# Optimization experiments

Measured on AMD Instinct MI355X. Metric: run time of the kernel, lower is better.

The kernel has to match this reference:

```python
import jax, jax.numpy as jnp
import numpy as np
from jax import lax

EPOCHS = 3
N_IN, N_OUT = 20, 18
BN_EPS = 1e-5
RECT_EPS = 1e-4
TRIU = np.triu_indices(N_OUT)  # SPDVectorize upper-triangular indices


def _orth(key, n, m):
    # Stiefel init: orthonormal columns, like nn.init.orthogonal_
    q, _ = jnp.linalg.qr(jax.random.normal(key, (n, m), dtype=jnp.float32))
    return q


def setup_inputs() -> dict:
    key = jax.random.key(0)
    ks = jax.random.split(key, 8)
    bs = 2048
    f32 = jnp.float32
    return dict(
        x=jax.random.normal(ks[0], (bs, 1, 22, 438), dtype=f32),
        W1=jax.random.normal(ks[1], (22, 1, 22, 1), dtype=f32) * 0.1,
        b1=jnp.zeros((22,), f32),
        g1=jnp.ones((22,), f32), be1=jnp.zeros((22,), f32),
        W2=jax.random.normal(ks[2], (20, 22, 1, 12), dtype=f32) * 0.05,
        b2=jnp.zeros((20,), f32),
        g2=jnp.ones((20,), f32), be2=jnp.zeros((20,), f32),
        Wq=_orth(ks[3], N_IN, N_OUT),
        Wk=_orth(ks[4], N_IN, N_OUT),
        Wv=_orth(ks[5], N_IN, N_OUT),
        Wl=jax.random.normal(ks[6], (N_OUT * (N_OUT + 1) // 2 * EPOCHS, 4), dtype=f32) * 0.02,
        bl=jnp.zeros((4,), f32),
    )


def _bn(x, g, b):
    # BatchNorm2d forward in training mode (batch statistics, biased var)
    mean = x.mean(axis=(0, 2, 3), keepdims=True)
    var = ((x - mean) ** 2).mean(axis=(0, 2, 3), keepdims=True)
    return (x - mean) * lax.rsqrt(var + BN_EPS) * g[None, :, None, None] + b[None, :, None, None]


def _conv(x, w, b, pad_w):
    y = lax.conv_general_dilated(x, w, (1, 1), [(0, 0), (pad_w, pad_w)],
                                 dimension_numbers=('NCHW', 'OIHW', 'NCHW'))
    return y + b[None, :, None, None]


def _signal2spd(x):
    # x: (bs, C, L) -> trace-normalized covariance + 1e-5 * I
    L = x.shape[-1]
    xc = x - x.mean(-1, keepdims=True)
    cov = jnp.einsum('bcl,bdl->bcd', xc, xc) / (L - 1)
    cov = cov / jnp.trace(cov, axis1=-2, axis2=-1)[:, None, None]
    return cov + 1e-5 * jnp.eye(cov.shape[-1], dtype=cov.dtype)


def _patch_lens(n, epochs):
    base = n // epochs
    lens = [base] * epochs
    for i in range(n - base * epochs):
        lens[i] += 1
    return lens


def _spd_fn(t, fn):
    # SPD functional calculus via eigh (== torch.svd on SPD input)
    s, u = jnp.linalg.eigh(t)
    return jnp.einsum('...ij,...j,...kj->...ik', u, fn(s), u)


def _forward(x, W1, b1, g1, be1, W2, b2, g2, be2, Wq, Wk, Wv, Wl, bl):
    bs = x.shape[0]
    h = _bn(_conv(x, W1, b1, 0), g1, be1)          # (bs,22,1,438)
    h = _bn(_conv(h, W2, b2, 6), g2, be2)          # (bs,20,1,439)
    sig = h[:, :, 0, :]                            # squeeze -> (bs,20,439)
    covs, off = [], 0
    for L in _patch_lens(sig.shape[-1], EPOCHS):   # E2R: [147,146,146]
        covs.append(_signal2spd(sig[:, :, off:off + L]))
        off += L
    X = jnp.stack(covs, axis=1)                    # (bs,m,20,20) SPD
    # SPDTransform: W^T X W with Stiefel W (20,18)
    Q = jnp.einsum('pi,bmpq,qj->bmij', Wq, X, Wq)
    K = jnp.einsum('pi,bmpq,qj->bmij', Wk, X, Wk)
    V = jnp.einsum('pi,bmpq,qj->bmij', Wv, X, Wv)
    logQ = _spd_fn(Q, jnp.log)
    logK = _spd_fn(K, jnp.log)
    logV = _spd_fn(V, jnp.log)
    # log-Euclidean distance^2: ||log Q_j - log K_i||_F^2  (== sum of svd singvals of D D^T)
    diff = logQ[:, :, None] - logK[:, None, :]     # (bs, mq, mk, n, n)
    energy = jnp.sum(diff * diff, axis=(-2, -1))   # (bs, mq, mk)
    scores = 1.0 / (1.0 + jnp.log1p(energy))
    # torch: softmax over dim=-2 then permute(0,2,1) == softmax over K index here
    P = jax.nn.softmax(scores, axis=-1)            # (bs, mq, mk)
    mixed = jnp.einsum('bji,bipq->bjpq', P, logV)  # weighted log-Euclidean mean
    out = _spd_fn(mixed, jnp.exp)
    out = _spd_fn(out, lambda s: jnp.maximum(s, RECT_EPS))  # SPDRectified
    logO = _spd_fn(out, jnp.log)                   # SPDTangentSpace log
    vec = logO[..., TRIU[0], TRIU[1]]              # (bs, m, 171)
    return vec.reshape(bs, -1) @ Wl + bl           # (bs, 4)


def reference(x, W1, b1, g1, be1, W2, b2, g2, be2, Wq, Wk, Wv, Wl, bl):
    return _forward(x, W1, b1, g1, be1, W2, b2, g2, be2, Wq, Wk, Wv, Wl, bl)
```

## Files before the change

### kernel.cpp

```cpp
#include <hip/hip_runtime.h>
#include <math.h>

#define OFF_Y2   0
#define OFF_QKV  17981440
#define OFF_ST   (17981440 + 5971968)
#define ST_SX   0
#define ST_SXX  22
#define ST_WF   506
#define ST_BF   990
#define ST_Y2S  1012
#define ST_Y2Q  1032
#define ST_TOT  1052

#define LOGEPS -9.210340371976182f
#define NSWEEP 5
#define SHIFT  12.0f

__global__ __launch_bounds__(256) void k0_zero(float* __restrict__ st){
  for (int i = threadIdx.x; i < ST_TOT; i += 256) st[i] = 0.f;
}

__global__ __launch_bounds__(256) void k1_xstats(const float* __restrict__ x, float* __restrict__ st){
  __shared__ __align__(16) float xs[22*444];
  const float* xb = x + (size_t)blockIdx.x * (22*438);
  for (int i = threadIdx.x; i < 22*444; i += 256){
    int h = i / 444, w = i - h*444;
    xs[i] = (w < 438) ? xb[h*438 + w] : 0.f;
  }
  __syncthreads();
  for (int t = threadIdx.x; t < 275; t += 256){
    if (t < 22){
      const float4* r = (const float4*)&xs[t*444];
      float4 acc = {0.f,0.f,0.f,0.f};
      for (int w = 0; w < 111; ++w){ float4 v = r[w]; acc.x+=v.x; acc.y+=v.y; acc.z+=v.z; acc.w+=v.w; }
      atomicAdd(&st[ST_SX + t], acc.x+acc.y+acc.z+acc.w);
    } else {
      int rem = t - 22, h = 0;
      while (rem >= 22 - h){ rem -= 22 - h; ++h; }
      int h2 = h + rem;
      const float4* ra = (const float4*)&xs[h*444];
      const float4* rb = (const float4*)&xs[h2*444];
      float4 acc = {0.f,0.f,0.f,0.f};
      for (int w = 0; w < 111; ++w){
        float4 a = ra[w], b = rb[w];
        acc.x = fmaf(a.x,b.x,acc.x); acc.y = fmaf(a.y,b.y,acc.y);
        acc.z = fmaf(a.z,b.z,acc.z); acc.w = fmaf(a.w,b.w,acc.w);
      }
      atomicAdd(&st[ST_SXX + h*22 + h2], acc.x+acc.y+acc.z+acc.w);
    }
  }
}

__global__ __launch_bounds__(64) void k1b_fold(const float* __restrict__ W1, const float* __restrict__ g1,
                                               const float* __restrict__ be1, float* __restrict__ st){
  int c = threadIdx.x;
  if (c >= 22) return;
  const float invN = 1.f / (2048.f*438.f);
  float mcol[22];
  float mu0 = 0.f;
  for (int h = 0; h < 22; ++h){ mcol[h] = W1[c*22 + h]; mu0 = fmaf(mcol[h], st[ST_SX + h], mu0); }
  mu0 *= invN;
  float qf = 0.f;
  for (int h = 0; h < 22; ++h)
    for (int h2 = h; h2 < 22; ++h2){
      float w = mcol[h]*mcol[h2]*st[ST_SXX + h*22 + h2];
      qf += (h2 == h) ? w : 2.f*w;
    }
  qf *= invN;
  float var = qf - mu0*mu0;
  float a1 = g1[c] * rsqrtf(var + 1e-5f);
  for (int h = 0; h < 22; ++h) st[ST_WF + h*22 + c] = a1 * mcol[h];
  st[ST_BF + c] = be1[c] - a1 * mu0;
}

__global__ __launch_bounds__(256) void k2_weff(const float* __restrict__ W2, const float* __restrict__ st,
                                               float* __restrict__ weff2, float* __restrict__ pfx){
  __shared__ float wf[484];
  __shared__ float bf[22];
  for (int i = threadIdx.x; i < 484; i += 256) wf[i] = st[ST_WF + i];
  if (threadIdx.x < 22) bf[threadIdx.x] = st[ST_BF + threadIdx.x];
  __syncthreads();
  for (int i = threadIdx.x; i < 5280; i += 256){
    int t = i % 12; int tmp = i / 12;
    int dl = tmp % 5; tmp /= 5;
    int h = tmp % 22; int dg = tmp / 22;
    int d = dg*5 + dl;
    float a = 0.f;
    for (int c = 0; c < 22; ++c) a = fmaf(W2[d*264 + c*12 + t], wf[h*22 + c], a);
    weff2[i] = a;
  }
  if (threadIdx.x < 20){
    int d = threadIdx.x;
    float run = 0.f;
    pfx[d*13 + 0] = 0.f;
    for (int t = 0; t < 12; ++t){
      float a = 0.f;
      for (int c = 0; c < 22; ++c) a = fmaf(W2[d*264 + c*12 + t], bf[c], a);
      run += a;
      pfx[d*13 + t + 1] = run;
    }
  }
}

__global__ __launch_bounds__(512, 3) void k3_conv(const float* __restrict__ x,
    const float* __restrict__ weff2, const float* __restrict__ pfx,
    float* __restrict__ st, float* __restrict__ y2){
  __shared__ __align__(16) float xs[22*452];
  __shared__ float ps[260];
  __shared__ float sloc[20], qloc[20];
  int tid = threadIdx.x;
  int n = blockIdx.x;
  const float* xb = x + (size_t)n*9636;
  for (int i = tid; i < 22*452; i += 512){
    int h = i / 452, w = i - h*452;
    int gx = w - 6;
    xs[i] = (gx >= 0 && gx < 438) ? xb[h*438 + gx] : 0.f;
  }
  if (tid < 260) ps[tid] = pfx[tid];
  if (tid < 40){ if (tid < 20) sloc[tid] = 0.f; else qloc[tid-20] = 0.f; }
  __syncthreads();
  int wave = tid >> 6;
  int dg = __builtin_amdgcn_readfirstlane(wave >> 1);
  int ct = tid & 127;
  bool act = ct < 110;
  int c0 = act ? ct*4 : 0;
  float acc[5][4];
  #pragma unroll
  for (int dl = 0; dl < 5; ++dl)
    #pragma unroll
    for (int j = 0; j < 4; ++j) acc[dl][j] = 0.f;
  const float* wb = weff2 + dg*1320;
  #pragma unroll 1
  for (int h = 0; h < 22; ++h){
    const float4* xr = (const float4*)&xs[h*452 + c0];
    float4 v0 = xr[0], v1 = xr[1], v2 = xr[2], v3 = xr[3];
    float xw[16] = {v0.x,v0.y,v0.z,v0.w, v1.x,v1.y,v1.z,v1.w,
                    v2.x,v2.y,v2.z,v2.w, v3.x,v3.y,v3.z,v3.w};
    const float* wp = wb + h*60;
    #pragma unroll
    for (int dl = 0; dl < 5; ++dl){
      #pragma unroll
      for (int t = 0; t < 12; ++t){
        float w = wp[dl*12 + t];
        #pragma unroll
        for (int j = 0; j < 4; ++j)
          acc[dl][j] = fmaf(w, xw[t+j], acc[dl][j]);
      }
    }
  }
  float s5[5], q5[5];
  #pragma unroll
  for (int dl = 0; dl < 5; ++dl){ s5[dl] = 0.f; q5[dl] = 0.f; }
  if (act){
    #pragma unroll
    for (int dl = 0; dl < 5; ++dl){
      int d = dg*5 + dl;
      float* yb = y2 + (size_t)n*8780 + (size_t)d*439;
      #pragma unroll
      for (int j = 0; j < 4; ++j){
        int gw = c0 + j;
        if (gw < 439){
          int lo = 6 - gw; if (lo < 0) lo = 0;
          int hi = 444 - gw; if (hi > 12) hi = 12;
          float val = acc[dl][j] + (ps[d*13 + hi] - ps[d*13 + lo]);
          yb[gw] = val;
          s5[dl] += val; q5[dl] = fmaf(val, val, q5[dl]);
        }
      }
    }
  }
  #pragma unroll
  for (int off = 32; off; off >>= 1){
    #pragma unroll
    for (int dl = 0; dl < 5; ++dl){
      s5[dl] += __shfl_down(s5[dl], off);
      q5[dl] += __shfl_down(q5[dl], off);
    }
  }
  if ((tid & 63) == 0){
    #pragma unroll
    for (int dl = 0; dl < 5; ++dl){
      atomicAdd(&sloc[dg*5 + dl], s5[dl]);
      atomicAdd(&qloc[dg*5 + dl], q5[dl]);
    }
  }
  __syncthreads();
  if (tid < 20){
    atomicAdd(&st[ST_Y2S + tid], sloc[tid]);
    atomicAdd(&st[ST_Y2Q + tid], qloc[tid]);
  }
}

__global__ __launch_bounds__(256) void k4_cov_qkv(const float* __restrict__ y2, const float* __restrict__ st,
    const float* __restrict__ g2, const float* __restrict__ Wq, const float* __restrict__ Wk,
    const float* __restrict__ Wv, float* __restrict__ qkv){
  __shared__ __align__(16) float ysp[3][20][148];
  __shared__ float a2s[20];
  __shared__ __align__(16) float Bt[3][18][20];
  __shared__ __align__(16) float G3[3][400];
  __shared__ __align__(16) float Tmt[3][360];
  __shared__ float musum3[3][20];
  __shared__ float rtr3[3];
  int tid = threadIdx.x, n = blockIdx.x;
  if (tid < 20){
    const float invN = 1.f/(2048.f*439.f);
    float s = st[ST_Y2S + tid]*invN;
    float q = st[ST_Y2Q + tid]*invN;
    a2s[tid] = g2[tid] * rsqrtf(q - s*s + 1e-5f);
  }
  const float* yb = y2 + (size_t)n*8780;
  for (int i = tid; i < 8780; i += 256){
    int d = i/439, w = i - d*439;
    int m = (w >= 293) ? 2 : ((w >= 147) ? 1 : 0);
    int lw = w - ((m == 2) ? 293 : ((m == 1) ? 147 : 0));
    ysp[m][d][lw] = yb[i];
  }
  if (tid < 100){
    int d = tid/5, k = tid - d*5;
    int m = (k == 0) ? 0 : ((k < 3) ? 1 : 2);
    int lw = (k == 0) ? 147 : ((k == 1 || k == 3) ? 146 : 147);
    ysp[m][d][lw] = 0.f;
  }
  __syncthreads();
  for (int i = tid; i < 1140; i += 256){
    if (i < 1080){
      int wt = i/360, r = i - wt*360; int d = r/18, jj = r - d*18;
      const float* Wm = (wt==0) ? Wq : ((wt==1) ? Wk : Wv);
      Bt[wt][jj][d] = a2s[d]*Wm[d*18 + jj];
    } else {
      int t = i - 1080; int m = t/20, d = t - m*20;
      const float4* r = (const float4*)&ysp[m][d][0];
      float4 acc = {0.f,0.f,0.f,0.f};
      #pragma unroll 1
      for (int w = 0; w < 37; ++w){ float4 v = r[w]; acc.x+=v.x; acc.y+=v.y; acc.z+=v.z; acc.w+=v.w; }
      musum3[m][d] = acc.x+acc.y+acc.z+acc.w;
    }
  }
  __syncthreads();
  for (int it = tid; it < 630; it += 256){
    int m = it/210, t = it - m*210;
    int rem = t, c = 0;
    while (rem >= 20 - c){ rem -= 20 - c; ++c; }
    int d = c + rem;
    const float4* ra = (const float4*)&ysp[m][c][0];
    const float4* rb = (const float4*)&ysp[m][d][0];
    float4 acc4 = {0.f,0.f,0.f,0.f};
    #pragma unroll 1
    for (int w = 0; w < 37; ++w){
      float4 a = ra[w], b = rb[w];
      acc4.x = fmaf(a.x,b.x,acc4.x); acc4.y = fmaf(a.y,b.y,acc4.y);
      acc4.z = fmaf(a.z,b.z,acc4.z); acc4.w = fmaf(a.w,b.w,acc4.w);
    }
    float invL = (m == 0) ? (1.f/147.f) : (1.f/146.f);
    float acc = (acc4.x+acc4.y+acc4.z+acc4.w) - musum3[m][c]*musum3[m][d]*invL;
    G3[m][c*20 + d] = acc; G3[m][d*20 + c] = acc;
  }
  __syncthreads();
  for (int wt = 0; wt < 3; ++wt){
    for (int i = tid; i < 1083; i += 256){
      if (i < 1080){
        int m = i/360, r = i - m*360; int p = r/18, jj = r - p*18;
        const float4* gr = (const float4*)&G3[m][p*20];
        const float4* br = (const float4*)&Bt[wt][jj][0];
        float4 a4 = {0.f,0.f,0.f,0.f};
        #pragma unroll
        for (int w = 0; w < 5; ++w){
          float4 a = gr[w], b = br[w];
          a4.x = fmaf(a.x,b.x,a4.x); a4.y = fmaf(a.y,b.y,a4.y);
          a4.z = fmaf(a.z,b.z,a4.z); a4.w = fmaf(a.w,b.w,a4.w);
        }
        Tmt[m][jj*20 + p] = a4.x+a4.y+a4.z+a4.w;
      } else if (wt == 0){
        int m = i - 1080;
        float tr = 0.f;
        for (int c = 0; c < 20; ++c){ float a = a2s[c]; tr = fmaf(a*a, G3[m][c*21], tr); }
        rtr3[m] = 1.f/tr;
      }
    }
    __syncthreads();
    for (int it = tid; it < 513; it += 256){
      int m = it/171, t = it - m*171;
      int rem = t, i = 0;
      while (rem >= 18 - i){ rem -= 18 - i; ++i; }
      int jj = i + rem;
      const float4* br = (const float4*)&Bt[wt][i][0];
      const float4* tr = (const float4*)&Tmt[m][jj*20];
      float4 a4 = {0.f,0.f,0.f,0.f};
      #pragma unroll
      for (int w = 0; w < 5; ++w){
        float4 a = br[w], b = tr[w];
        a4.x = fmaf(a.x,b.x,a4.x); a4.y = fmaf(a.y,b.y,a4.y);
        a4.z = fmaf(a.z,b.z,a4.z); a4.w = fmaf(a.w,b.w,a4.w);
      }
      float acc = (a4.x+a4.y+a4.z+a4.w) * rtr3[m];
      if (i == jj) acc += 1e-5f;
      float* outm = qkv + ((size_t)wt*6144 + (size_t)n*3 + m)*324;
      outm[i*18 + jj] = acc; outm[jj*18 + i] = acc;
    }
    __syncthreads();
  }
}

__global__ __launch_bounds__(256, 4) void k5_oneside(const float* __restrict__ src, float* __restrict__ dst,
    int nmat, int mode, const float* __restrict__ Wl, const float* __restrict__ bl,
    float* __restrict__ outp){
  __shared__ __align__(16) float stage[12][384];
  __shared__ __align__(16) float wls[2052];
  __shared__ float outacc[4][4];
  int tid = threadIdx.x;
  int wave = tid >> 6, lane = tid & 63;
  int g = (lane >= 54) ? 3 : (lane >= 36 ? 2 : (lane >= 18 ? 1 : 0));
  int j = lane - g*18;
  int gb = g*18;
  int slot = wave*3 + ((g < 3) ? g : 0);
  int mat = blockIdx.x*12 + wave*3 + g;
  bool act = (g < 3) && (mat < nmat);

  if (mode == 1){
    for (int i = tid; i < 2052; i += 256) wls[i] = Wl[i];
    if (tid < 16) outacc[tid >> 2][tid & 3] = 0.f;
  }

  float b[18];
  float sh = (mode == 1) ? SHIFT : 0.f;
  if (act){
    const float* s = src + (size_t)mat*324 + j*18;
    #pragma unroll
    for (int i = 0; i < 18; ++i) b[i] = s[i] + ((i == j) ? sh : 0.f);
  } else {
    #pragma unroll
    for (int i = 0; i < 18; ++i) b[i] = (i == j) ? 1.f : 0.f;
  }
  float nrm;
  { float n0 = 0.f, n1 = 0.f;
    #pragma unroll
    for (int k = 0; k < 18; k += 2){ n0 = fmaf(b[k],b[k],n0); n1 = fmaf(b[k+1],b[k+1],n1); }
    nrm = n0 + n1; }

  #pragma unroll 1
  for (int sweep = 0; sweep < NSWEEP; ++sweep){
    #pragma unroll
    for (int r = 0; r < 17; ++r){
      int xx = j - 1 - r; if (xx < 0) xx += 17;
      int v = r + 17 - xx; if (v >= 17) v -= 17;
      int m = (j == 0) ? (1 + r) : ((xx == 0) ? 0 : (1 + v));
      bool isp = (j == 0) ? true : ((xx == 0) ? false : (xx <= 8));
      int plane = (gb + m) & 63;
      float rv[18];
      #pragma unroll
      for (int k = 0; k < 18; ++k) rv[k] = __shfl(b[k], plane);
      float on = __shfl(nrm, plane);
      float g0 = 0.f, g1 = 0.f;
      #pragma unroll
      for (int k = 0; k < 18; k += 2){ g0 = fmaf(b[k], rv[k], g0); g1 = fmaf(b[k+1], rv[k+1], g1); }
      float gam = g0 + g1;
      float alpha = isp ? nrm : on;
      float beta  = isp ? on  : nrm;
      float tau = (beta - alpha) * 0.5f * __builtin_amdgcn_rcpf(gam);
      float tt = __builtin_amdgcn_rcpf(fabsf(tau) + sqrtf(fmaf(tau, tau, 1.f)));
      float t = (tau >= 0.f) ? tt : -tt;
      if (!(fabsf(gam) > 1e-36f)) t = 0.f;
      float c = __builtin_amdgcn_rsqf(fmaf(t, t, 1.f));
      float s = t*c;
      nrm = fmaf(isp ? -t : t, gam, nrm);
      float sg = isp ? -s : s;
      #pragma unroll
      for (int k = 0; k < 18; ++k) b[k] = fmaf(c, b[k], sg*rv[k]);
    }
  }
  float n0 = 0.f, n1 = 0.f;
  #pragma unroll
  for (int k = 0; k < 18; k += 2){ n0 = fmaf(b[k],b[k],n0); n1 = fmaf(b[k+1],b[k+1],n1); }
  float nf = fmaxf(n0 + n1, 1e-30f);
  float fv = (mode == 0) ? (0.5f * logf(nf)) : fmaxf(sqrtf(nf) - SHIFT, LOGEPS);
  float wv = fv * __builtin_amdgcn_rcpf(nf);
  float* sp = &stage[slot][0];
  if (act){
    #pragma unroll
    for (int k = 0; k < 18; ++k) sp[k*20 + j] = b[k];
    sp[360 + j] = wv;
  }
  __syncthreads();
  if (act){
    float wr[18];
    #pragma unroll
    for (int i = 0; i < 18; ++i) wr[i] = sp[j*20 + i] * sp[360 + i];
    float frow[18];
    #pragma unroll
    for (int i2 = 0; i2 < 18; ++i2){
      const float* br = &sp[i2*20];
      float a0 = 0.f;
      #pragma unroll
      for (int k = 0; k < 16; k += 4){
        float4 v4 = *(const float4*)&br[k];
        a0 = fmaf(wr[k],   v4.x, a0); a0 = fmaf(wr[k+1], v4.y, a0);
        a0 = fmaf(wr[k+2], v4.z, a0); a0 = fmaf(wr[k+3], v4.w, a0);
      }
      a0 = fmaf(wr[16], br[16], a0);
      a0 = fmaf(wr[17], br[17], a0);
      frow[i2] = a0;
    }
    if (mode == 0){
      float* orow = dst + (size_t)mat*324 + j*18;
      #pragma unroll
      for (int i2 = 0; i2 < 18; ++i2) orow[i2] = frow[i2];
    } else {
      int base = (g*171 + j*(37 - j)/2 - j)*4;
      float o0=0.f, o1=0.f, o2=0.f, o3=0.f;
      #pragma unroll
      for (int jj = 0; jj < 18; ++jj){
        if (jj >= j){
          const float* w4 = &wls[base + jj*4];
          o0 = fmaf(frow[jj], w4[0], o0);
          o1 = fmaf(frow[jj], w4[1], o1);
          o2 = fmaf(frow[jj], w4[2], o2);
          o3 = fmaf(frow[jj], w4[3], o3);
        }
      }
      atomicAdd(&outacc[wave][0], o0);
      atomicAdd(&outacc[wave][1], o1);
      atomicAdd(&outacc[wave][2], o2);
      atomicAdd(&outacc[wave][3], o3);
    }
  }
  if (mode == 1){
    __syncthreads();
    if (tid < 16){
      int bi = tid >> 2, o = tid & 3;
      outp[(blockIdx.x*4 + bi)*4 + o] = outacc[bi][o] + bl[o];
    }
  }
}

__global__ __launch_bounds__(128) void k6_attnmix(const float* __restrict__ logs, float* __restrict__ mixed){
  __shared__ float lq[972], lk[972], lv[972];
  __shared__ float ew[2][9];
  __shared__ float P[9];
  int b = blockIdx.x, tid = threadIdx.x;
  const float* q  = logs + (size_t)b*972;
  const float* k_ = logs + 1990656 + (size_t)b*972;
  const float* v_ = logs + 3981312 + (size_t)b*972;
  for (int i = tid; i < 972; i += 128){ lq[i] = q[i]; lk[i] = k_[i]; lv[i] = v_[i]; }
  __syncthreads();
  float e[9] = {0.f,0.f,0.f,0.f,0.f,0.f,0.f,0.f,0.f};
  for (int x = tid; x < 324; x += 128){
    float q0 = lq[x], q1 = lq[324+x], q2 = lq[648+x];
    float k0 = lk[x], k1 = lk[324+x], k2 = lk[648+x];
    float d;
    d = q0-k0; e[0] = fmaf(d,d,e[0]);
    d = q0-k1; e[1] = fmaf(d,d,e[1]);
    d = q0-k2; e[2] = fmaf(d,d,e[2]);
    d = q1-k0; e[3] = fmaf(d,d,e[3]);
    d = q1-k1; e[4] = fmaf(d,d,e[4]);
    d = q1-k2; e[5] = fmaf(d,d,e[5]);
    d = q2-k0; e[6] = fmaf(d,d,e[6]);
    d = q2-k1; e[7] = fmaf(d,d,e[7]);
    d = q2-k2; e[8] = fmaf(d,d,e[8]);
  }
  #pragma unroll
  for (int p = 0; p < 9; ++p)
    for (int off = 32; off; off >>= 1) e[p] += __shfl_down(e[p], off);
  if ((tid & 63) == 0){
    #pragma unroll
    for (int p = 0; p < 9; ++p) ew[tid >> 6][p] = e[p];
  }
  __syncthreads();
  if (tid < 3){
    float en0 = ew[0][tid*3+0] + ew[1][tid*3+0];
    float en1 = ew[0][tid*3+1] + ew[1][tid*3+1];
    float en2 = ew[0][tid*3+2] + ew[1][tid*3+2];
    float s0 = 1.f/(1.f + log1pf(en0));
    float s1 = 1.f/(1.f + log1pf(en1));
    float s2 = 1.f/(1.f + log1pf(en2));
    float mx = fmaxf(s0, fmaxf(s1, s2));
    float e0 = expf(s0-mx), e1 = expf(s1-mx), e2 = expf(s2-mx);
    float inv = 1.f/(e0+e1+e2);
    P[tid*3+0] = e0*inv; P[tid*3+1] = e1*inv; P[tid*3+2] = e2*inv;
  }
  __syncthreads();
  float p00=P[0],p01=P[1],p02=P[2],p10=P[3],p11=P[4],p12=P[5],p20=P[6],p21=P[7],p22=P[8];
  float* mb = mixed + (size_t)b*972;
  for (int x = tid; x < 324; x += 128){
    float v0 = lv[x], v1 = lv[324+x], v2 = lv[648+x];
    mb[x]     = p00*v0 + p01*v1 + p02*v2;
    mb[324+x] = p10*v0 + p11*v1 + p12*v2;
    mb[648+x] = p20*v0 + p21*v1 + p22*v2;
  }
}

extern "C" void kernel_launch(void* const* d_in, const int* in_sizes, int n_in,
                              void* d_out, int out_size, void* d_ws, size_t ws_size,
                              hipStream_t stream){
  (void)in_sizes; (void)n_in; (void)out_size; (void)ws_size;
  const float* x   = (const float*)d_in[0];
  const float* W1  = (const float*)d_in[1];
  const float* g1  = (const float*)d_in[3];
  const float* be1 = (const float*)d_in[4];
  const float* W2  = (const float*)d_in[5];
  const float* g2  = (const float*)d_in[7];
  const float* Wq  = (const float*)d_in[9];
  const float* Wk  = (const float*)d_in[10];
  const float* Wv  = (const float*)d_in[11];
  const float* Wl  = (const float*)d_in[12];
  const float* bl  = (const float*)d_in[13];
  float* ws    = (float*)d_ws;
  float* y2    = ws + OFF_Y2;
  float* qkv   = ws + OFF_QKV;
  float* weff2 = ws + OFF_QKV;
  float* pfx   = ws + OFF_QKV + 5280;
  float* logs  = ws + OFF_Y2;
  float* mixed = ws + OFF_QKV;
  float* st    = ws + OFF_ST;
  float* outp  = (float*)d_out;

  k0_zero    <<<dim3(1),       dim3(256), 0, stream>>>(st);
  k1_xstats  <<<dim3(2048),    dim3(256), 0, stream>>>(x, st);
  k1b_fold   <<<dim3(1),       dim3(64),  0, stream>>>(W1, g1, be1, st);
  k2_weff    <<<dim3(1),       dim3(256), 0, stream>>>(W2, st, weff2, pfx);
  k3_conv    <<<dim3(2048),    dim3(512), 0, stream>>>(x, weff2, pfx, st, y2);
  k4_cov_qkv <<<dim3(2048),    dim3(256), 0, stream>>>(y2, st, g2, Wq, Wk, Wv, qkv);
  k5_oneside <<<dim3(1536),    dim3(256), 0, stream>>>(qkv, logs, 18432, 0, nullptr, nullptr, nullptr);
  k6_attnmix <<<dim3(2048),    dim3(128), 0, stream>>>(logs, mixed);
  k5_oneside <<<dim3(512),     dim3(256), 0, stream>>>(mixed, nullptr, 6144, 1, Wl, bl, outp);
}
```

Baseline: 659.4 us.

## Fuse per-patch covariance Gram computation into the conv kernel

The conv kernel now keeps its outputs in shared memory, reusing the input tile buffer, and computes the three per-patch centered Gram matrices there. It writes only 1200 floats per sample instead of the full 8780-float conv output. The downstream kernel just loads these Gram matrices, which removes a large global write and read of the intermediate activation. The conv kernel gains a few barriers and the Gram loop uses only 630 of its 512-thread block's work items.

```diff
diff --git a/kernel.cpp b/kernel.cpp
--- a/kernel.cpp
+++ b/kernel.cpp
@@ -1,7 +1,7 @@
 #include <hip/hip_runtime.h>
 #include <math.h>
 
-#define OFF_Y2   0
+#define OFF_G3   0
 #define OFF_QKV  17981440
 #define OFF_ST   (17981440 + 5971968)
 #define ST_SX   0
@@ -102,19 +102,21 @@
   }
 }
 
-__global__ __launch_bounds__(512, 3) void k3_conv(const float* __restrict__ x,
+__global__ __launch_bounds__(512, 3) void k3_convg(const float* __restrict__ x,
     const float* __restrict__ weff2, const float* __restrict__ pfx,
-    float* __restrict__ st, float* __restrict__ y2){
-  __shared__ __align__(16) float xs[22*452];
-  __shared__ float ps[260];
-  __shared__ float sloc[20], qloc[20];
+    float* __restrict__ st, float* __restrict__ g3o){
+  __shared__ __align__(16) float smem[10304];
+  float* ps   = smem + 9944;
+  float* sloc = smem + 10204;
+  float* qloc = smem + 10224;
+  float* mus  = smem + 10244;
   int tid = threadIdx.x;
   int n = blockIdx.x;
   const float* xb = x + (size_t)n*9636;
   for (int i = tid; i < 22*452; i += 512){
     int h = i / 452, w = i - h*452;
     int gx = w - 6;
-    xs[i] = (gx >= 0 && gx < 438) ? xb[h*438 + gx] : 0.f;
+    smem[i] = (gx >= 0 && gx < 438) ? xb[h*438 + gx] : 0.f;
   }
   if (tid < 260) ps[tid] = pfx[tid];
   if (tid < 40){ if (tid < 20) sloc[tid] = 0.f; else qloc[tid-20] = 0.f; }
@@ -132,7 +134,7 @@
   const float* wb = weff2 + dg*1320;
   #pragma unroll 1
   for (int h = 0; h < 22; ++h){
-    const float4* xr = (const float4*)&xs[h*452 + c0];
+    const float4* xr = (const float4*)&smem[h*452 + c0];
     float4 v0 = xr[0], v1 = xr[1], v2 = xr[2], v3 = xr[3];
     float xw[16] = {v0.x,v0.y,v0.z,v0.w, v1.x,v1.y,v1.z,v1.w,
                     v2.x,v2.y,v2.z,v2.w, v3.x,v3.y,v3.z,v3.w};
@@ -155,7 +157,6 @@
     #pragma unroll
     for (int dl = 0; dl < 5; ++dl){
       int d = dg*5 + dl;
-      float* yb = y2 + (size_t)n*8780 + (size_t)d*439;
       #pragma unroll
       for (int j = 0; j < 4; ++j){
         int gw = c0 + j;
@@ -163,7 +164,7 @@
           int lo = 6 - gw; if (lo < 0) lo = 0;
           int hi = 444 - gw; if (hi > 12) hi = 12;
           float val = acc[dl][j] + (ps[d*13 + hi] - ps[d*13 + lo]);
-          yb[gw] = val;
+          acc[dl][j] = val;
           s5[dl] += val; q5[dl] = fmaf(val, val, q5[dl]);
         }
       }
@@ -189,17 +190,65 @@
     atomicAdd(&st[ST_Y2S + tid], sloc[tid]);
     atomicAdd(&st[ST_Y2Q + tid], qloc[tid]);
   }
-}
-
-__global__ __launch_bounds__(256) void k4_cov_qkv(const float* __restrict__ y2, const float* __restrict__ st,
+  if (act){
+    #pragma unroll
+    for (int dl = 0; dl < 5; ++dl){
+      int d = dg*5 + dl;
+      #pragma unroll
+      for (int j = 0; j < 4; ++j){
+        int gw = c0 + j;
+        if (gw < 439){
+          int m = (gw >= 293) ? 2 : ((gw >= 147) ? 1 : 0);
+          int lw = gw - ((m == 2) ? 293 : ((m == 1) ? 147 : 0));
+          smem[m*2960 + d*148 + lw] = acc[dl][j];
+        }
+      }
+    }
+  }
+  if (tid < 100){
+    int d = tid/5, k = tid - d*5;
+    int m = (k == 0) ? 0 : ((k < 3) ? 1 : 2);
+    int lw = (k == 0) ? 147 : ((k == 1 || k == 3) ? 146 : 147);
+    smem[m*2960 + d*148 + lw] = 0.f;
+  }
+  __syncthreads();
+  if (tid < 60){
+    int m = tid/20, d = tid - m*20;
+    const float4* r = (const float4*)&smem[m*2960 + d*148];
+    float4 a4 = {0.f,0.f,0.f,0.f};
+    #pragma unroll 1
+    for (int w = 0; w < 37; ++w){ float4 v = r[w]; a4.x+=v.x; a4.y+=v.y; a4.z+=v.z; a4.w+=v.w; }
+    mus[tid] = a4.x+a4.y+a4.z+a4.w;
+  }
+  __syncthreads();
+  for (int it = tid; it < 630; it += 512){
+    int m = it/210, t = it - m*210;
+    int rem = t, c = 0;
+    while (rem >= 20 - c){ rem -= 20 - c; ++c; }
+    int d = c + rem;
+    const float4* ra = (const float4*)&smem[m*2960 + c*148];
+    const float4* rb = (const float4*)&smem[m*2960 + d*148];
+    float4 acc4 = {0.f,0.f,0.f,0.f};
+    #pragma unroll 1
+    for (int w = 0; w < 37; ++w){
+      float4 a = ra[w], b = rb[w];
+      acc4.x = fmaf(a.x,b.x,acc4.x); acc4.y = fmaf(a.y,b.y,acc4.y);
+      acc4.z = fmaf(a.z,b.z,acc4.z); acc4.w = fmaf(a.w,b.w,acc4.w);
+    }
+    float invL = (m == 0) ? (1.f/147.f) : (1.f/146.f);
+    float a = (acc4.x+acc4.y+acc4.z+acc4.w) - mus[m*20+c]*mus[m*20+d]*invL;
+    float* gm = g3o + (size_t)n*1200 + m*400;
+    gm[c*20 + d] = a; gm[d*20 + c] = a;
+  }
+}
+
+__global__ __launch_bounds__(256) void k4_qkv(const float* __restrict__ g3i, const float* __restrict__ st,
     const float* __restrict__ g2, const float* __restrict__ Wq, const float* __restrict__ Wk,
     const float* __restrict__ Wv, float* __restrict__ qkv){
-  __shared__ __align__(16) float ysp[3][20][148];
+  __shared__ __align__(16) float G3[3][400];
   __shared__ float a2s[20];
   __shared__ __align__(16) float Bt[3][18][20];
-  __shared__ __align__(16) float G3[3][400];
   __shared__ __align__(16) float Tmt[3][360];
-  __shared__ float musum3[3][20];
   __shared__ float rtr3[3];
   int tid = threadIdx.x, n = blockIdx.x;
   if (tid < 20){
@@ -208,52 +257,13 @@
     float q = st[ST_Y2Q + tid]*invN;
     a2s[tid] = g2[tid] * rsqrtf(q - s*s + 1e-5f);
   }
-  const float* yb = y2 + (size_t)n*8780;
-  for (int i = tid; i < 8780; i += 256){
-    int d = i/439, w = i - d*439;
-    int m = (w >= 293) ? 2 : ((w >= 147) ? 1 : 0);
-    int lw = w - ((m == 2) ? 293 : ((m == 1) ? 147 : 0));
-    ysp[m][d][lw] = yb[i];
-  }
-  if (tid < 100){
-    int d = tid/5, k = tid - d*5;
-    int m = (k == 0) ? 0 : ((k < 3) ? 1 : 2);
-    int lw = (k == 0) ? 147 : ((k == 1 || k == 3) ? 146 : 147);
-    ysp[m][d][lw] = 0.f;
-  }
-  __syncthreads();
-  for (int i = tid; i < 1140; i += 256){
-    if (i < 1080){
-      int wt = i/360, r = i - wt*360; int d = r/18, jj = r - d*18;
-      const float* Wm = (wt==0) ? Wq : ((wt==1) ? Wk : Wv);
-      Bt[wt][jj][d] = a2s[d]*Wm[d*18 + jj];
-    } else {
-      int t = i - 1080; int m = t/20, d = t - m*20;
-      const float4* r = (const float4*)&ysp[m][d][0];
-      float4 acc = {0.f,0.f,0.f,0.f};
-      #pragma unroll 1
-      for (int w = 0; w < 37; ++w){ float4 v = r[w]; acc.x+=v.x; acc.y+=v.y; acc.z+=v.z; acc.w+=v.w; }
-      musum3[m][d] = acc.x+acc.y+acc.z+acc.w;
-    }
-  }
-  __syncthreads();
-  for (int it = tid; it < 630; it += 256){
-    int m = it/210, t = it - m*210;
-    int rem = t, c = 0;
-    while (rem >= 20 - c){ rem -= 20 - c; ++c; }
-    int d = c + rem;
-    const float4* ra = (const float4*)&ysp[m][c][0];
-    const float4* rb = (const float4*)&ysp[m][d][0];
-    float4 acc4 = {0.f,0.f,0.f,0.f};
-    #pragma unroll 1
-    for (int w = 0; w < 37; ++w){
-      float4 a = ra[w], b = rb[w];
-      acc4.x = fmaf(a.x,b.x,acc4.x); acc4.y = fmaf(a.y,b.y,acc4.y);
-      acc4.z = fmaf(a.z,b.z,acc4.z); acc4.w = fmaf(a.w,b.w,acc4.w);
-    }
-    float invL = (m == 0) ? (1.f/147.f) : (1.f/146.f);
-    float acc = (acc4.x+acc4.y+acc4.z+acc4.w) - musum3[m][c]*musum3[m][d]*invL;
-    G3[m][c*20 + d] = acc; G3[m][d*20 + c] = acc;
+  const float* gi = g3i + (size_t)n*1200;
+  for (int i = tid; i < 1200; i += 256) (&G3[0][0])[i] = gi[i];
+  __syncthreads();
+  for (int i = tid; i < 1080; i += 256){
+    int wt = i/360, r = i - wt*360; int d = r/18, jj = r - d*18;
+    const float* Wm = (wt==0) ? Wq : ((wt==1) ? Wk : Wv);
+    Bt[wt][jj][d] = a2s[d]*Wm[d*18 + jj];
   }
   __syncthreads();
   for (int wt = 0; wt < 3; ++wt){
@@ -504,11 +514,11 @@
   const float* Wl  = (const float*)d_in[12];
   const float* bl  = (const float*)d_in[13];
   float* ws    = (float*)d_ws;
-  float* y2    = ws + OFF_Y2;
+  float* g3buf = ws + OFF_G3;
   float* qkv   = ws + OFF_QKV;
   float* weff2 = ws + OFF_QKV;
   float* pfx   = ws + OFF_QKV + 5280;
-  float* logs  = ws + OFF_Y2;
+  float* logs  = ws + OFF_G3;
   float* mixed = ws + OFF_QKV;
   float* st    = ws + OFF_ST;
   float* outp  = (float*)d_out;
@@ -517,8 +527,8 @@
   k1_xstats  <<<dim3(2048),    dim3(256), 0, stream>>>(x, st);
   k1b_fold   <<<dim3(1),       dim3(64),  0, stream>>>(W1, g1, be1, st);
   k2_weff    <<<dim3(1),       dim3(256), 0, stream>>>(W2, st, weff2, pfx);
-  k3_conv    <<<dim3(2048),    dim3(512), 0, stream>>>(x, weff2, pfx, st, y2);
-  k4_cov_qkv <<<dim3(2048),    dim3(256), 0, stream>>>(y2, st, g2, Wq, Wk, Wv, qkv);
+  k3_convg   <<<dim3(2048),    dim3(512), 0, stream>>>(x, weff2, pfx, st, g3buf);
+  k4_qkv     <<<dim3(2048),    dim3(256), 0, stream>>>(g3buf, st, g2, Wq, Wk, Wv, qkv);
   k5_oneside <<<dim3(1536),    dim3(256), 0, stream>>>(qkv, logs, 18432, 0, nullptr, nullptr, nullptr);
   k6_attnmix <<<dim3(2048),    dim3(128), 0, stream>>>(logs, mixed);
   k5_oneside <<<dim3(512),     dim3(256), 0, stream>>>(mixed, nullptr, 6144, 1, Wl, bl, outp);
```

New measurement: 695.3 us. 1.05x slower.
